# Kernel tuning notes

Hardware: AMD Instinct MI355X
Metric: run time of the kernel (lower is better)

Reference implementation:

```python
import jax, jax.numpy as jnp
import numpy as np

N_NODES = 100000
N_EDGES = 800000
IN_DIM = 128
HIDDEN = 128
CLASSES = 40


def _glorot(key, shape):
    fan_in, fan_out = shape
    lim = (6.0 / (fan_in + fan_out)) ** 0.5
    return jax.random.uniform(key, shape, jnp.float32, -lim, lim)


def setup_inputs() -> dict:
    key = jax.random.key(0)
    ks = jax.random.split(key, 8)
    x = jax.random.normal(ks[0], (N_NODES, IN_DIM), jnp.float32)
    edge_index = jax.random.randint(ks[1], (2, N_EDGES), 0, N_NODES, jnp.int64)
    # SAGEConv layer 1: lin_l (neighbor, with bias), lin_r (root, no bias)
    W1_l = _glorot(ks[2], (IN_DIM, HIDDEN))
    W1_r = _glorot(ks[3], (IN_DIM, HIDDEN))
    b1 = jnp.zeros((HIDDEN,), jnp.float32)
    # SAGEConv layer 2
    W2_l = _glorot(ks[4], (HIDDEN, CLASSES))
    W2_r = _glorot(ks[5], (HIDDEN, CLASSES))
    b2 = jnp.zeros((CLASSES,), jnp.float32)
    return {"x": x, "edge_index": edge_index, "W1_l": W1_l, "W1_r": W1_r,
            "b1": b1, "W2_l": W2_l, "W2_r": W2_r, "b2": b2}


def _sage_conv(x, src, dst, W_l, W_r, b):
    # mean aggregation of source-node features into destination nodes
    msgs = x[src]                                             # [E, d] gather
    agg = jax.ops.segment_sum(msgs, dst, num_segments=N_NODES)  # [N, d]
    cnt = jax.ops.segment_sum(jnp.ones((src.shape[0],), x.dtype), dst,
                              num_segments=N_NODES)           # [N]
    mean = agg / jnp.maximum(cnt, 1.0)[:, None]
    return mean @ W_l + x @ W_r + b


def reference(x, edge_index, W1_l, W1_r, b1, W2_l, W2_r, b2):
    src, dst = edge_index[0], edge_index[1]
    h = _sage_conv(x, src, dst, W1_l, W1_r, b1)
    h = jax.nn.relu(h)
    # F.dropout in eval mode is the identity (deterministic reference)
    out = _sage_conv(h, src, dst, W2_l, W2_r, b2)
    return out
```

## Files before the change

kernel.cpp:

```cpp
#include <hip/hip_runtime.h>
#include <hip/hip_bf16.h>

#define N_NODES 100000
#define N_EDGES 800000
#define IN_DIM  128
#define HIDDEN  128
#define CLASSES 40
#define CAP     32
#define NSH     8
#define SLICES  100
#define EPB     8000
#define BIN_B   (NSH*SLICES)
#define CAST_B  12500
#define PACK_B  24
#define CUR_STRIDE 12544

typedef __attribute__((ext_vector_type(8))) short bf16x8;
typedef __attribute__((ext_vector_type(4))) float floatx4;

__device__ __forceinline__ float bf2f(unsigned short u) {
    return __uint_as_float(((unsigned int)u) << 16);
}
__device__ __forceinline__ unsigned short f2bf(float f) {
    unsigned int u = __float_as_uint(f);
    unsigned int r = 0x7fffu + ((u >> 16) & 1u);
    return (unsigned short)((u + r) >> 16);
}
__device__ __forceinline__ int curIdx(int d) { return (d & 7) * CUR_STRIDE + (d >> 3); }

__global__ void k_prep(const int* __restrict__ src, const int* __restrict__ dst,
                       int* __restrict__ cur, int* __restrict__ csr,
                       const float* __restrict__ x, unsigned short* __restrict__ Xbf,
                       const float* __restrict__ W1l, const float* __restrict__ W1r,
                       unsigned short* __restrict__ Bp1,
                       const float* __restrict__ W2l, const float* __restrict__ W2r,
                       unsigned short* __restrict__ Bp2) {
    int blk = blockIdx.x;
    if (blk < BIN_B) {
        int g = blk & 7;
        int slice = blk >> 3;
        const int4* s4p = reinterpret_cast<const int4*>(src) + slice * (EPB / 4);
        const int4* d4p = reinterpret_cast<const int4*>(dst) + slice * (EPB / 4);
        for (int i = threadIdx.x; i < EPB / 4; i += 256) {
            int4 d4 = d4p[i];
            int4 s4 = s4p[i];
            #pragma unroll
            for (int j = 0; j < 4; ++j) {
                int d = (&d4.x)[j];
                if ((d & 7) == g) {
                    int s = (&s4.x)[j];
                    int slot = atomicAdd(&cur[g * CUR_STRIDE + (d >> 3)], 1);
                    if (slot < CAP) csr[d * CAP + slot] = s;
                }
            }
        }
    } else if (blk < BIN_B + CAST_B) {
        int t = (blk - BIN_B) * 256 + threadIdx.x;
        int n = t >> 5, g = t & 31;
        float4 v = reinterpret_cast<const float4*>(x + (size_t)n * 128)[g];
        ushort4 u = { f2bf(v.x), f2bf(v.y), f2bf(v.z), f2bf(v.w) };
        *(ushort4*)(Xbf + (size_t)n * 128 + g * 4) = u;
    } else {
        int t = (blk - BIN_B - CAST_B) * 256 + threadIdx.x;
        if (t < 4096) {
            int o = t >> 7, n = t & 127;
            const float* W = (o < 16) ? W1l : W1r;
            int k0 = (o & 15) * 8;
            union { unsigned short us[8]; uint4 v; } pk;
            #pragma unroll
            for (int j = 0; j < 8; ++j) pk.us[j] = f2bf(W[(size_t)(k0 + j) * 128 + n]);
            *(uint4*)(Bp1 + (size_t)t * 8) = pk.v;
        } else {
            int t2 = t - 4096;
            int o = t2 >> 7, n = t2 & 127;
            const float* W = (n < 64) ? W2l : W2r;
            int col = n & 63;
            int k0 = o * 8;
            union { unsigned short us[8]; uint4 v; } pk;
            #pragma unroll
            for (int j = 0; j < 8; ++j)
                pk.us[j] = (col < 40) ? f2bf(W[(size_t)(k0 + j) * 40 + col]) : (unsigned short)0;
            *(uint4*)(Bp2 + (size_t)t2 * 8) = pk.v;
        }
    }
}

__global__ void k_agg1(const unsigned short* __restrict__ Xbf,
                       unsigned short* __restrict__ Mean,
                       const int* __restrict__ deg, const int* __restrict__ csr) {
    int n = blockIdx.x * 4 + (threadIdx.x >> 6);
    int lane = threadIdx.x & 63;
    if (n >= N_NODES) return;
    int cnt = min(deg[curIdx(n)], CAP);
    int nl = csr[n * CAP + (lane & (CAP - 1))];
    int r = lane >> 4, c = lane & 15;
    float acc[8] = {0.f, 0.f, 0.f, 0.f, 0.f, 0.f, 0.f, 0.f};
    for (int base = 0; base < cnt; base += 8) {
        #pragma unroll
        for (int u = 0; u < 2; ++u) {
            int e = base + u * 4 + r;
            int s = __shfl(nl, min(e, cnt - 1) & 31, 64);
            bf16x8 v = {};
            if (e < cnt)
                v = *(const bf16x8*)(Xbf + (size_t)s * 128 + c * 8);
            #pragma unroll
            for (int j = 0; j < 8; ++j) acc[j] += bf2f((unsigned short)v[j]);
        }
    }
    #pragma unroll
    for (int j = 0; j < 8; ++j) {
        acc[j] += __shfl_xor(acc[j], 16, 64);
        acc[j] += __shfl_xor(acc[j], 32, 64);
    }
    if (lane < 16) {
        float inv = 1.0f / fmaxf((float)cnt, 1.0f);
        union { unsigned short us[8]; bf16x8 v; } pk;
        #pragma unroll
        for (int j = 0; j < 8; ++j) pk.us[j] = f2bf(acc[j] * inv);
        *(bf16x8*)(Mean + (size_t)n * 128 + c * 8) = pk.v;
    }
}

__global__ __launch_bounds__(256)
void k_gemm(const unsigned short* __restrict__ Mean, const unsigned short* __restrict__ Xbf,
            unsigned short* __restrict__ Pbuf, unsigned short* __restrict__ Rbuf,
            const unsigned short* __restrict__ Bp1, const float* __restrict__ b1,
            const unsigned short* __restrict__ Bp2) {
    __shared__ unsigned short Hs[4][16][136];
    int wv = threadIdx.x >> 6, lane = threadIdx.x & 63;
    int q = lane >> 4, nn = lane & 15;
    int m0 = blockIdx.x * 64 + wv * 16;
    int ma = m0 + nn;
    bool mv = (ma < N_NODES);

    bf16x8 a_all[8];
    #pragma unroll
    for (int kt = 0; kt < 8; ++kt) {
        const unsigned short* tab = (kt < 4) ? Mean : Xbf;
        bf16x8 a = {};
        if (mv) a = *(const bf16x8*)(tab + (size_t)ma * 128 + (kt & 3) * 32 + q * 8);
        a_all[kt] = a;
    }

    floatx4 acc[8] = {};
    #pragma unroll
    for (int kt = 0; kt < 8; ++kt) {
        bf16x8 b[8];
        #pragma unroll
        for (int nt = 0; nt < 8; ++nt)
            b[nt] = *(const bf16x8*)(Bp1 + ((size_t)((kt * 4 + q) * 128 + nt * 16 + nn)) * 8);
        #pragma unroll
        for (int nt = 0; nt < 8; ++nt)
            acc[nt] = __builtin_amdgcn_mfma_f32_16x16x32_bf16(a_all[kt], b[nt], acc[nt], 0, 0, 0);
    }
    #pragma unroll
    for (int nt = 0; nt < 8; ++nt) {
        int col = nt * 16 + nn;
        float bias = b1[col];
        #pragma unroll
        for (int r = 0; r < 4; ++r)
            Hs[wv][q * 4 + r][col] = f2bf(fmaxf(acc[nt][r] + bias, 0.f));
    }
    floatx4 acc2[8] = {};
    #pragma unroll
    for (int kt = 0; kt < 4; ++kt) {
        bf16x8 a = *(const bf16x8*)(&Hs[wv][nn][kt * 32 + q * 8]);
        bf16x8 b[8];
        #pragma unroll
        for (int nt = 0; nt < 8; ++nt)
            b[nt] = *(const bf16x8*)(Bp2 + ((size_t)((kt * 4 + q) * 128 + nt * 16 + nn)) * 8);
        #pragma unroll
        for (int nt = 0; nt < 8; ++nt)
            acc2[nt] = __builtin_amdgcn_mfma_f32_16x16x32_bf16(a, b[nt], acc2[nt], 0, 0, 0);
    }
    #pragma unroll
    for (int nt = 0; nt < 4; ++nt) {
        int col = nt * 16 + nn;
        #pragma unroll
        for (int r = 0; r < 4; ++r) {
            int ro = m0 + q * 4 + r;
            if (ro < N_NODES)
                Pbuf[(size_t)ro * 64 + col] = f2bf(acc2[nt][r]);
        }
    }
    #pragma unroll
    for (int nt = 4; nt < 8; ++nt) {
        int col = (nt - 4) * 16 + nn;
        #pragma unroll
        for (int r = 0; r < 4; ++r) {
            int ro = m0 + q * 4 + r;
            if (ro < N_NODES)
                Rbuf[(size_t)ro * 64 + col] = f2bf(acc2[nt][r]);
        }
    }
}

__global__ void k_agg2(const unsigned short* __restrict__ Pbuf,
                       const unsigned short* __restrict__ Rbuf,
                       const int* __restrict__ deg, const int* __restrict__ csr,
                       const float* __restrict__ b2, float* __restrict__ out) {
    int n = blockIdx.x * 4 + (threadIdx.x >> 6);
    int lane = threadIdx.x & 63;
    if (n >= N_NODES) return;
    int cnt = min(deg[curIdx(n)], CAP);
    int nl = csr[n * CAP + (lane & (CAP - 1))];
    int r = lane >> 3, c = lane & 7;
    float acc[8] = {0.f, 0.f, 0.f, 0.f, 0.f, 0.f, 0.f, 0.f};
    for (int base = 0; base < cnt; base += 8) {
        int e = base + r;
        int s = __shfl(nl, min(e, cnt - 1) & 31, 64);
        bf16x8 v = {};
        if (e < cnt)
            v = *(const bf16x8*)(Pbuf + (size_t)s * 64 + c * 8);
        #pragma unroll
        for (int j = 0; j < 8; ++j) acc[j] += bf2f((unsigned short)v[j]);
    }
    #pragma unroll
    for (int j = 0; j < 8; ++j) {
        acc[j] += __shfl_xor(acc[j], 8, 64);
        acc[j] += __shfl_xor(acc[j], 16, 64);
        acc[j] += __shfl_xor(acc[j], 32, 64);
    }
    if (lane < 5) {
        float inv = 1.0f / fmaxf((float)cnt, 1.0f);
        bf16x8 rv = *(const bf16x8*)(Rbuf + (size_t)n * 64 + c * 8);
        float o[8];
        #pragma unroll
        for (int j = 0; j < 8; ++j)
            o[j] = acc[j] * inv + bf2f((unsigned short)rv[j]) + b2[c * 8 + j];
        float* op = out + (size_t)n * CLASSES + c * 8;
        *(float4*)(op)     = make_float4(o[0], o[1], o[2], o[3]);
        *(float4*)(op + 4) = make_float4(o[4], o[5], o[6], o[7]);
    }
}

extern "C" void kernel_launch(void* const* d_in, const int* in_sizes, int n_in,
                              void* d_out, int out_size, void* d_ws, size_t ws_size,
                              hipStream_t stream) {
    const float* x   = (const float*)d_in[0];
    const int*   ei  = (const int*)d_in[1];
    const float* W1l = (const float*)d_in[2];
    const float* W1r = (const float*)d_in[3];
    const float* b1  = (const float*)d_in[4];
    const float* W2l = (const float*)d_in[5];
    const float* W2r = (const float*)d_in[6];
    const float* b2  = (const float*)d_in[7];
    float* out = (float*)d_out;

    const int* src = ei;
    const int* dst = ei + N_EDGES;

    char* ws = (char*)d_ws;
    size_t off = 0;
    auto alloc = [&](size_t bytes) { void* p = ws + off; off += (bytes + 511) & ~(size_t)511; return p; };
    int* cur = (int*)alloc((size_t)NSH * CUR_STRIDE * 4);
    int* csr = (int*)alloc((size_t)N_NODES * CAP * 4);
    unsigned short* Bp1 = (unsigned short*)alloc((size_t)32 * 128 * 8 * 2);
    unsigned short* Bp2 = (unsigned short*)alloc((size_t)16 * 128 * 8 * 2);
    unsigned short* Xbf  = (unsigned short*)alloc((size_t)N_NODES * 128 * 2);
    unsigned short* Mean = (unsigned short*)alloc((size_t)N_NODES * 128 * 2);
    unsigned short* Pbuf = (unsigned short*)alloc((size_t)N_NODES * 64 * 2);
    unsigned short* Rbuf = (unsigned short*)alloc((size_t)N_NODES * 64 * 2);

    hipMemsetAsync(cur, 0, (size_t)NSH * CUR_STRIDE * 4, stream);

    k_prep<<<BIN_B + CAST_B + PACK_B, 256, 0, stream>>>(
        src, dst, cur, csr, x, Xbf, W1l, W1r, Bp1, W2l, W2r, Bp2);

    k_agg1<<<(N_NODES + 3) / 4, 256, 0, stream>>>(Xbf, Mean, cur, csr);
    k_gemm<<<(N_NODES + 63) / 64, 256, 0, stream>>>(Mean, Xbf, Pbuf, Rbuf, Bp1, b1, Bp2);
    k_agg2<<<(N_NODES + 3) / 4, 256, 0, stream>>>(Pbuf, Rbuf, cur, csr, b2, out);
}
```

Baseline: 249.3 us.

## Fuse all stages into one persistent cooperative kernel with grid syncs

Replaces the memset and four separate kernel launches with a single cooperative persistent kernel. Blocks grid-stride over each stage's former block indices, and grid.sync separates the phases. This is meant to remove launch and inter-kernel gaps. In exchange it caps occupancy via launch_bounds, uses a fixed grid of 256 CUs times blocks-per-CU, and adds grid-wide barrier costs. The GEMM stage's register pressure may also now limit occupancy for the gather phases.

After: 956.0 us. 3.84x slower.

```diff
diff --git a/kernel.cpp b/kernel.cpp
--- a/kernel.cpp
+++ b/kernel.cpp
@@ -1,5 +1,8 @@
 #include <hip/hip_runtime.h>
 #include <hip/hip_bf16.h>
+#include <hip/hip_cooperative_groups.h>
+
+namespace cg = cooperative_groups;
 
 #define N_NODES 100000
 #define N_EDGES 800000
@@ -13,6 +16,9 @@
 #define BIN_B   (NSH*SLICES)
 #define CAST_B  12500
 #define PACK_B  24
+#define PREP_B  (BIN_B + CAST_B + PACK_B)
+#define AGG_B   ((N_NODES + 3) / 4)
+#define GEMM_B  ((N_NODES + 63) / 64)
 #define CUR_STRIDE 12544
 
 typedef __attribute__((ext_vector_type(8))) short bf16x8;
@@ -28,209 +34,226 @@
 }
 __device__ __forceinline__ int curIdx(int d) { return (d & 7) * CUR_STRIDE + (d >> 3); }
 
-__global__ void k_prep(const int* __restrict__ src, const int* __restrict__ dst,
-                       int* __restrict__ cur, int* __restrict__ csr,
-                       const float* __restrict__ x, unsigned short* __restrict__ Xbf,
-                       const float* __restrict__ W1l, const float* __restrict__ W1r,
-                       unsigned short* __restrict__ Bp1,
-                       const float* __restrict__ W2l, const float* __restrict__ W2r,
-                       unsigned short* __restrict__ Bp2) {
-    int blk = blockIdx.x;
-    if (blk < BIN_B) {
-        int g = blk & 7;
-        int slice = blk >> 3;
-        const int4* s4p = reinterpret_cast<const int4*>(src) + slice * (EPB / 4);
-        const int4* d4p = reinterpret_cast<const int4*>(dst) + slice * (EPB / 4);
-        for (int i = threadIdx.x; i < EPB / 4; i += 256) {
-            int4 d4 = d4p[i];
-            int4 s4 = s4p[i];
-            #pragma unroll
-            for (int j = 0; j < 4; ++j) {
-                int d = (&d4.x)[j];
-                if ((d & 7) == g) {
-                    int s = (&s4.x)[j];
-                    int slot = atomicAdd(&cur[g * CUR_STRIDE + (d >> 3)], 1);
-                    if (slot < CAP) csr[d * CAP + slot] = s;
+__global__ __launch_bounds__(256, 5)
+void k_all(const int* __restrict__ src, const int* __restrict__ dst,
+           int* __restrict__ cur, int* __restrict__ csr,
+           const float* __restrict__ x, unsigned short* __restrict__ Xbf,
+           const float* __restrict__ W1l, const float* __restrict__ W1r,
+           unsigned short* __restrict__ Bp1, const float* __restrict__ b1,
+           const float* __restrict__ W2l, const float* __restrict__ W2r,
+           unsigned short* __restrict__ Bp2,
+           unsigned short* __restrict__ Mean, unsigned short* __restrict__ Pbuf,
+           unsigned short* __restrict__ Rbuf,
+           const float* __restrict__ b2, float* __restrict__ out)
+{
+    cg::grid_group grid = cg::this_grid();
+    const int nb   = gridDim.x;
+    const int bid  = blockIdx.x;
+    const int tid  = threadIdx.x;
+    const int lane = tid & 63;
+    const int wv   = tid >> 6;
+    __shared__ unsigned short Hs[4][16][136];
+
+    for (int i = bid * 256 + tid; i < NSH * CUR_STRIDE; i += nb * 256) cur[i] = 0;
+    __threadfence();
+    grid.sync();
+
+    for (int blk = bid; blk < PREP_B; blk += nb) {
+        if (blk < BIN_B) {
+            int g = blk & 7;
+            int slice = blk >> 3;
+            const int4* s4p = reinterpret_cast<const int4*>(src) + slice * (EPB / 4);
+            const int4* d4p = reinterpret_cast<const int4*>(dst) + slice * (EPB / 4);
+            for (int i = tid; i < EPB / 4; i += 256) {
+                int4 d4 = d4p[i];
+                int4 s4 = s4p[i];
+                #pragma unroll
+                for (int j = 0; j < 4; ++j) {
+                    int d = (&d4.x)[j];
+                    if ((d & 7) == g) {
+                        int s = (&s4.x)[j];
+                        int slot = atomicAdd(&cur[g * CUR_STRIDE + (d >> 3)], 1);
+                        if (slot < CAP) csr[d * CAP + slot] = s;
+                    }
                 }
             }
+        } else if (blk < BIN_B + CAST_B) {
+            int t = (blk - BIN_B) * 256 + tid;
+            int n = t >> 5, gg = t & 31;
+            float4 v = reinterpret_cast<const float4*>(x + (size_t)n * 128)[gg];
+            ushort4 u = { f2bf(v.x), f2bf(v.y), f2bf(v.z), f2bf(v.w) };
+            *(ushort4*)(Xbf + (size_t)n * 128 + gg * 4) = u;
+        } else {
+            int t = (blk - BIN_B - CAST_B) * 256 + tid;
+            if (t < 4096) {
+                int o = t >> 7, n = t & 127;
+                const float* W = (o < 16) ? W1l : W1r;
+                int k0 = (o & 15) * 8;
+                union { unsigned short us[8]; uint4 v; } pk;
+                #pragma unroll
+                for (int j = 0; j < 8; ++j) pk.us[j] = f2bf(W[(size_t)(k0 + j) * 128 + n]);
+                *(uint4*)(Bp1 + (size_t)t * 8) = pk.v;
+            } else {
+                int t2 = t - 4096;
+                int o = t2 >> 7, n = t2 & 127;
+                const float* W = (n < 64) ? W2l : W2r;
+                int col = n & 63;
+                int k0 = o * 8;
+                union { unsigned short us[8]; uint4 v; } pk;
+                #pragma unroll
+                for (int j = 0; j < 8; ++j)
+                    pk.us[j] = (col < 40) ? f2bf(W[(size_t)(k0 + j) * 40 + col]) : (unsigned short)0;
+                *(uint4*)(Bp2 + (size_t)t2 * 8) = pk.v;
+            }
         }
-    } else if (blk < BIN_B + CAST_B) {
-        int t = (blk - BIN_B) * 256 + threadIdx.x;
-        int n = t >> 5, g = t & 31;
-        float4 v = reinterpret_cast<const float4*>(x + (size_t)n * 128)[g];
-        ushort4 u = { f2bf(v.x), f2bf(v.y), f2bf(v.z), f2bf(v.w) };
-        *(ushort4*)(Xbf + (size_t)n * 128 + g * 4) = u;
-    } else {
-        int t = (blk - BIN_B - CAST_B) * 256 + threadIdx.x;
-        if (t < 4096) {
-            int o = t >> 7, n = t & 127;
-            const float* W = (o < 16) ? W1l : W1r;
-            int k0 = (o & 15) * 8;
-            union { unsigned short us[8]; uint4 v; } pk;
-            #pragma unroll
-            for (int j = 0; j < 8; ++j) pk.us[j] = f2bf(W[(size_t)(k0 + j) * 128 + n]);
-            *(uint4*)(Bp1 + (size_t)t * 8) = pk.v;
-        } else {
-            int t2 = t - 4096;
-            int o = t2 >> 7, n = t2 & 127;
-            const float* W = (n < 64) ? W2l : W2r;
-            int col = n & 63;
-            int k0 = o * 8;
-            union { unsigned short us[8]; uint4 v; } pk;
-            #pragma unroll
-            for (int j = 0; j < 8; ++j)
-                pk.us[j] = (col < 40) ? f2bf(W[(size_t)(k0 + j) * 40 + col]) : (unsigned short)0;
-            *(uint4*)(Bp2 + (size_t)t2 * 8) = pk.v;
+    }
+    __threadfence();
+    grid.sync();
+
+    {
+        int r = lane >> 4, c = lane & 15;
+        for (int vb = bid; vb < AGG_B; vb += nb) {
+            int n = vb * 4 + wv;
+            if (n >= N_NODES) continue;
+            int cnt = min(cur[curIdx(n)], CAP);
+            int nl = csr[n * CAP + (lane & (CAP - 1))];
+            float acc[8] = {0.f, 0.f, 0.f, 0.f, 0.f, 0.f, 0.f, 0.f};
+            for (int base = 0; base < cnt; base += 8) {
+                #pragma unroll
+                for (int u = 0; u < 2; ++u) {
+                    int e = base + u * 4 + r;
+                    int s = __shfl(nl, min(e, cnt - 1) & 31, 64);
+                    bf16x8 v = {};
+                    if (e < cnt)
+                        v = *(const bf16x8*)(Xbf + (size_t)s * 128 + c * 8);
+                    #pragma unroll
+                    for (int j = 0; j < 8; ++j) acc[j] += bf2f((unsigned short)v[j]);
+                }
+            }
+            #pragma unroll
+            for (int j = 0; j < 8; ++j) {
+                acc[j] += __shfl_xor(acc[j], 16, 64);
+                acc[j] += __shfl_xor(acc[j], 32, 64);
+            }
+            if (lane < 16) {
+                float inv = 1.0f / fmaxf((float)cnt, 1.0f);
+                union { unsigned short us[8]; bf16x8 v; } pk;
+                #pragma unroll
+                for (int j = 0; j < 8; ++j) pk.us[j] = f2bf(acc[j] * inv);
+                *(bf16x8*)(Mean + (size_t)n * 128 + c * 8) = pk.v;
+            }
         }
     }
-}
-
-__global__ void k_agg1(const unsigned short* __restrict__ Xbf,
-                       unsigned short* __restrict__ Mean,
-                       const int* __restrict__ deg, const int* __restrict__ csr) {
-    int n = blockIdx.x * 4 + (threadIdx.x >> 6);
-    int lane = threadIdx.x & 63;
-    if (n >= N_NODES) return;
-    int cnt = min(deg[curIdx(n)], CAP);
-    int nl = csr[n * CAP + (lane & (CAP - 1))];
-    int r = lane >> 4, c = lane & 15;
-    float acc[8] = {0.f, 0.f, 0.f, 0.f, 0.f, 0.f, 0.f, 0.f};
-    for (int base = 0; base < cnt; base += 8) {
-        #pragma unroll
-        for (int u = 0; u < 2; ++u) {
-            int e = base + u * 4 + r;
-            int s = __shfl(nl, min(e, cnt - 1) & 31, 64);
-            bf16x8 v = {};
-            if (e < cnt)
-                v = *(const bf16x8*)(Xbf + (size_t)s * 128 + c * 8);
-            #pragma unroll
-            for (int j = 0; j < 8; ++j) acc[j] += bf2f((unsigned short)v[j]);
+    __threadfence();
+    grid.sync();
+
+    {
+        int q = lane >> 4, nn = lane & 15;
+        for (int vb = bid; vb < GEMM_B; vb += nb) {
+            int m0 = vb * 64 + wv * 16;
+            int ma = m0 + nn;
+            bool mv = (ma < N_NODES);
+
+            bf16x8 a_all[8];
+            #pragma unroll
+            for (int kt = 0; kt < 8; ++kt) {
+                const unsigned short* tab = (kt < 4) ? Mean : Xbf;
+                bf16x8 a = {};
+                if (mv) a = *(const bf16x8*)(tab + (size_t)ma * 128 + (kt & 3) * 32 + q * 8);
+                a_all[kt] = a;
+            }
+
+            floatx4 acc[8] = {};
+            #pragma unroll
+            for (int kt = 0; kt < 8; ++kt) {
+                bf16x8 b[8];
+                #pragma unroll
+                for (int nt = 0; nt < 8; ++nt)
+                    b[nt] = *(const bf16x8*)(Bp1 + ((size_t)((kt * 4 + q) * 128 + nt * 16 + nn)) * 8);
+                #pragma unroll
+                for (int nt = 0; nt < 8; ++nt)
+                    acc[nt] = __builtin_amdgcn_mfma_f32_16x16x32_bf16(a_all[kt], b[nt], acc[nt], 0, 0, 0);
+            }
+            #pragma unroll
+            for (int nt = 0; nt < 8; ++nt) {
+                int col = nt * 16 + nn;
+                float bias = b1[col];
+                #pragma unroll
+                for (int r = 0; r < 4; ++r)
+                    Hs[wv][q * 4 + r][col] = f2bf(fmaxf(acc[nt][r] + bias, 0.f));
+            }
+            floatx4 acc2[8] = {};
+            #pragma unroll
+            for (int kt = 0; kt < 4; ++kt) {
+                bf16x8 a = *(const bf16x8*)(&Hs[wv][nn][kt * 32 + q * 8]);
+                bf16x8 b[8];
+                #pragma unroll
+                for (int nt = 0; nt < 8; ++nt)
+                    b[nt] = *(const bf16x8*)(Bp2 + ((size_t)((kt * 4 + q) * 128 + nt * 16 + nn)) * 8);
+                #pragma unroll
+                for (int nt = 0; nt < 8; ++nt)
+                    acc2[nt] = __builtin_amdgcn_mfma_f32_16x16x32_bf16(a, b[nt], acc2[nt], 0, 0, 0);
+            }
+            #pragma unroll
+            for (int nt = 0; nt < 4; ++nt) {
+                int col = nt * 16 + nn;
+                #pragma unroll
+                for (int r = 0; r < 4; ++r) {
+                    int ro = m0 + q * 4 + r;
+                    if (ro < N_NODES)
+                        Pbuf[(size_t)ro * 64 + col] = f2bf(acc2[nt][r]);
+                }
+            }
+            #pragma unroll
+            for (int nt = 4; nt < 8; ++nt) {
+                int col = (nt - 4) * 16 + nn;
+                #pragma unroll
+                for (int r = 0; r < 4; ++r) {
+                    int ro = m0 + q * 4 + r;
+                    if (ro < N_NODES)
+                        Rbuf[(size_t)ro * 64 + col] = f2bf(acc2[nt][r]);
+                }
+            }
         }
     }
-    #pragma unroll
-    for (int j = 0; j < 8; ++j) {
-        acc[j] += __shfl_xor(acc[j], 16, 64);
-        acc[j] += __shfl_xor(acc[j], 32, 64);
-    }
-    if (lane < 16) {
-        float inv = 1.0f / fmaxf((float)cnt, 1.0f);
-        union { unsigned short us[8]; bf16x8 v; } pk;
-        #pragma unroll
-        for (int j = 0; j < 8; ++j) pk.us[j] = f2bf(acc[j] * inv);
-        *(bf16x8*)(Mean + (size_t)n * 128 + c * 8) = pk.v;
-    }
-}
-
-__global__ __launch_bounds__(256)
-void k_gemm(const unsigned short* __restrict__ Mean, const unsigned short* __restrict__ Xbf,
-            unsigned short* __restrict__ Pbuf, unsigned short* __restrict__ Rbuf,
-            const unsigned short* __restrict__ Bp1, const float* __restrict__ b1,
-            const unsigned short* __restrict__ Bp2) {
-    __shared__ unsigned short Hs[4][16][136];
-    int wv = threadIdx.x >> 6, lane = threadIdx.x & 63;
-    int q = lane >> 4, nn = lane & 15;
-    int m0 = blockIdx.x * 64 + wv * 16;
-    int ma = m0 + nn;
-    bool mv = (ma < N_NODES);
-
-    bf16x8 a_all[8];
-    #pragma unroll
-    for (int kt = 0; kt < 8; ++kt) {
-        const unsigned short* tab = (kt < 4) ? Mean : Xbf;
-        bf16x8 a = {};
-        if (mv) a = *(const bf16x8*)(tab + (size_t)ma * 128 + (kt & 3) * 32 + q * 8);
-        a_all[kt] = a;
-    }
-
-    floatx4 acc[8] = {};
-    #pragma unroll
-    for (int kt = 0; kt < 8; ++kt) {
-        bf16x8 b[8];
-        #pragma unroll
-        for (int nt = 0; nt < 8; ++nt)
-            b[nt] = *(const bf16x8*)(Bp1 + ((size_t)((kt * 4 + q) * 128 + nt * 16 + nn)) * 8);
-        #pragma unroll
-        for (int nt = 0; nt < 8; ++nt)
-            acc[nt] = __builtin_amdgcn_mfma_f32_16x16x32_bf16(a_all[kt], b[nt], acc[nt], 0, 0, 0);
-    }
-    #pragma unroll
-    for (int nt = 0; nt < 8; ++nt) {
-        int col = nt * 16 + nn;
-        float bias = b1[col];
-        #pragma unroll
-        for (int r = 0; r < 4; ++r)
-            Hs[wv][q * 4 + r][col] = f2bf(fmaxf(acc[nt][r] + bias, 0.f));
-    }
-    floatx4 acc2[8] = {};
-    #pragma unroll
-    for (int kt = 0; kt < 4; ++kt) {
-        bf16x8 a = *(const bf16x8*)(&Hs[wv][nn][kt * 32 + q * 8]);
-        bf16x8 b[8];
-        #pragma unroll
-        for (int nt = 0; nt < 8; ++nt)
-            b[nt] = *(const bf16x8*)(Bp2 + ((size_t)((kt * 4 + q) * 128 + nt * 16 + nn)) * 8);
-        #pragma unroll
-        for (int nt = 0; nt < 8; ++nt)
-            acc2[nt] = __builtin_amdgcn_mfma_f32_16x16x32_bf16(a, b[nt], acc2[nt], 0, 0, 0);
-    }
-    #pragma unroll
-    for (int nt = 0; nt < 4; ++nt) {
-        int col = nt * 16 + nn;
-        #pragma unroll
-        for (int r = 0; r < 4; ++r) {
-            int ro = m0 + q * 4 + r;
-            if (ro < N_NODES)
-                Pbuf[(size_t)ro * 64 + col] = f2bf(acc2[nt][r]);
+    __threadfence();
+    grid.sync();
+
+    {
+        int r = lane >> 3, c = lane & 7;
+        for (int vb = bid; vb < AGG_B; vb += nb) {
+            int n = vb * 4 + wv;
+            if (n >= N_NODES) continue;
+            int cnt = min(cur[curIdx(n)], CAP);
+            int nl = csr[n * CAP + (lane & (CAP - 1))];
+            float acc[8] = {0.f, 0.f, 0.f, 0.f, 0.f, 0.f, 0.f, 0.f};
+            for (int base = 0; base < cnt; base += 8) {
+                int e = base + r;
+                int s = __shfl(nl, min(e, cnt - 1) & 31, 64);
+                bf16x8 v = {};
+                if (e < cnt)
+                    v = *(const bf16x8*)(Pbuf + (size_t)s * 64 + c * 8);
+                #pragma unroll
+                for (int j = 0; j < 8; ++j) acc[j] += bf2f((unsigned short)v[j]);
+            }
+            #pragma unroll
+            for (int j = 0; j < 8; ++j) {
+                acc[j] += __shfl_xor(acc[j], 8, 64);
+                acc[j] += __shfl_xor(acc[j], 16, 64);
+                acc[j] += __shfl_xor(acc[j], 32, 64);
+            }
+            if (lane < 5) {
+                float inv = 1.0f / fmaxf((float)cnt, 1.0f);
+                bf16x8 rv = *(const bf16x8*)(Rbuf + (size_t)n * 64 + c * 8);
+                float o[8];
+                #pragma unroll
+                for (int j = 0; j < 8; ++j)
+                    o[j] = acc[j] * inv + bf2f((unsigned short)rv[j]) + b2[c * 8 + j];
+                float* op = out + (size_t)n * CLASSES + c * 8;
+                *(float4*)(op)     = make_float4(o[0], o[1], o[2], o[3]);
+                *(float4*)(op + 4) = make_float4(o[4], o[5], o[6], o[7]);
+            }
         }
-    }
-    #pragma unroll
-    for (int nt = 4; nt < 8; ++nt) {
-        int col = (nt - 4) * 16 + nn;
-        #pragma unroll
-        for (int r = 0; r < 4; ++r) {
-            int ro = m0 + q * 4 + r;
-            if (ro < N_NODES)
-                Rbuf[(size_t)ro * 64 + col] = f2bf(acc2[nt][r]);
-        }
-    }
-}
-
-__global__ void k_agg2(const unsigned short* __restrict__ Pbuf,
-                       const unsigned short* __restrict__ Rbuf,
-                       const int* __restrict__ deg, const int* __restrict__ csr,
-                       const float* __restrict__ b2, float* __restrict__ out) {
-    int n = blockIdx.x * 4 + (threadIdx.x >> 6);
-    int lane = threadIdx.x & 63;
-    if (n >= N_NODES) return;
-    int cnt = min(deg[curIdx(n)], CAP);
-    int nl = csr[n * CAP + (lane & (CAP - 1))];
-    int r = lane >> 3, c = lane & 7;
-    float acc[8] = {0.f, 0.f, 0.f, 0.f, 0.f, 0.f, 0.f, 0.f};
-    for (int base = 0; base < cnt; base += 8) {
-        int e = base + r;
-        int s = __shfl(nl, min(e, cnt - 1) & 31, 64);
-        bf16x8 v = {};
-        if (e < cnt)
-            v = *(const bf16x8*)(Pbuf + (size_t)s * 64 + c * 8);
-        #pragma unroll
-        for (int j = 0; j < 8; ++j) acc[j] += bf2f((unsigned short)v[j]);
-    }
-    #pragma unroll
-    for (int j = 0; j < 8; ++j) {
-        acc[j] += __shfl_xor(acc[j], 8, 64);
-        acc[j] += __shfl_xor(acc[j], 16, 64);
-        acc[j] += __shfl_xor(acc[j], 32, 64);
-    }
-    if (lane < 5) {
-        float inv = 1.0f / fmaxf((float)cnt, 1.0f);
-        bf16x8 rv = *(const bf16x8*)(Rbuf + (size_t)n * 64 + c * 8);
-        float o[8];
-        #pragma unroll
-        for (int j = 0; j < 8; ++j)
-            o[j] = acc[j] * inv + bf2f((unsigned short)rv[j]) + b2[c * 8 + j];
-        float* op = out + (size_t)n * CLASSES + c * 8;
-        *(float4*)(op)     = make_float4(o[0], o[1], o[2], o[3]);
-        *(float4*)(op + 4) = make_float4(o[4], o[5], o[6], o[7]);
     }
 }
 
@@ -262,12 +285,20 @@
     unsigned short* Pbuf = (unsigned short*)alloc((size_t)N_NODES * 64 * 2);
     unsigned short* Rbuf = (unsigned short*)alloc((size_t)N_NODES * 64 * 2);
 
-    hipMemsetAsync(cur, 0, (size_t)NSH * CUR_STRIDE * 4, stream);
-
-    k_prep<<<BIN_B + CAST_B + PACK_B, 256, 0, stream>>>(
-        src, dst, cur, csr, x, Xbf, W1l, W1r, Bp1, W2l, W2r, Bp2);
-
-    k_agg1<<<(N_NODES + 3) / 4, 256, 0, stream>>>(Xbf, Mean, cur, csr);
-    k_gemm<<<(N_NODES + 63) / 64, 256, 0, stream>>>(Mean, Xbf, Pbuf, Rbuf, Bp1, b1, Bp2);
-    k_agg2<<<(N_NODES + 3) / 4, 256, 0, stream>>>(Pbuf, Rbuf, cur, csr, b2, out);
+    static int s_grid = 0;
+    if (s_grid == 0) {
+        int perCU = 0;
+        if (hipOccupancyMaxActiveBlocksPerMultiprocessor(&perCU, k_all, 256, 0) != hipSuccess
+            || perCU < 1) perCU = 4;
+        if (perCU > 5) perCU = 5;
+        s_grid = perCU * 256;
+    }
+
+    void* args[] = { (void*)&src, (void*)&dst, (void*)&cur, (void*)&csr,
+                     (void*)&x, (void*)&Xbf, (void*)&W1l, (void*)&W1r,
+                     (void*)&Bp1, (void*)&b1, (void*)&W2l, (void*)&W2r,
+                     (void*)&Bp2, (void*)&Mean, (void*)&Pbuf, (void*)&Rbuf,
+                     (void*)&b2, (void*)&out };
+    (void)hipLaunchCooperativeKernel((const void*)k_all, dim3(s_grid), dim3(256),
+                                     args, 0, stream);
 }
```
